# Optimization experiments

Measured on AMD Instinct MI355X. Metric: run time of the kernel, lower is better.

The kernel has to match this reference:

```python
import jax, jax.numpy as jnp
import numpy as np

BOOST_STRENGTH = 1.0  # from init kwargs, already >= 0


def setup_inputs() -> dict:
    key = jax.random.key(0)
    k1, k2 = jax.random.split(key)
    B, C, H, W = 64, 128, 56, 56
    x = jax.random.normal(k1, (B, C, H, W), dtype=jnp.float32)
    # duty cycles are running activation frequencies in [0, 1]
    duty_cycles = jax.random.uniform(k2, (1, C, 1, 1), dtype=jnp.float32)
    k = 40141  # round(0.1 * C*H*W)
    return {"x": x, "duty_cycles": duty_cycles, "k": k}


def reference(x, duty_cycles, k):
    B = x.shape[0]
    n = x.shape[1] * x.shape[2] * x.shape[3]
    target_density = jnp.float32(k / n)
    # boosting only selects winners; original (unboosted) values are kept
    boost_factors = jnp.exp((target_density - duty_cycles) * BOOST_STRENGTH)
    boosted = (x * boost_factors).reshape(B, -1)   # [B, n]
    flat_x = x.reshape(B, -1)                      # [B, n]
    _, idx = jax.lax.top_k(boosted, k)             # [B, k]
    winners = jnp.take_along_axis(flat_x, idx, axis=1)  # original values at winning units
    res = jnp.zeros_like(flat_x).at[jnp.arange(B)[:, None], idx].set(winners)
    return res.reshape(x.shape)
```

## Files before the change

kernel.cpp:

```cpp
#include <hip/hip_runtime.h>
#include <stdint.h>

#define BB 64
#define CC 128
#define HW 3136
#define NPR (CC * HW)
#define NBINS 8192
#define BIN_SHIFT 19
#define KEY_LOW 0x7FFFFu
#define NF4 6272
#define F4CH 784

typedef float vf4 __attribute__((ext_vector_type(4)));

#define ROWMETA_OFF 512
#define COUNTER_OFF 2048
#define HIST_OFF 4096
#define CAND_OFF (HIST_OFF + (size_t)BB * NBINS * 4)

__device__ __forceinline__ uint32_t tokey(float b) {
    uint32_t u = __float_as_uint(b);
    return u ^ (uint32_t)(((int32_t)u >> 31) | 0x80000000);
}

__device__ __forceinline__ float boostf(const float* dc, int c, int K) {
    float td = (float)((double)K / (double)NPR);
    float d = td - dc[c];
    return (float)exp((double)d);
}

__global__ __launch_bounds__(256) void k_hist(const float* __restrict__ x,
                                              const float* __restrict__ dc,
                                              const int* __restrict__ kptr,
                                              uint32_t* __restrict__ hist) {
    __shared__ uint32_t lh[NBINS];
    __shared__ float sbf[8];
    for (int i = threadIdx.x; i < NBINS; i += 256) lh[i] = 0;
    if (threadIdx.x < 8) {
        int c0 = (blockIdx.x & 15) * 8;
        sbf[threadIdx.x] = boostf(dc, c0 + threadIdx.x, *kptr);
    }
    __syncthreads();

    int row = blockIdx.x >> 4;
    int c0 = (blockIdx.x & 15) * 8;
    const float4* xp = (const float4*)(x + (size_t)row * NPR + (size_t)c0 * HW);

#define HPROC(av, tv)                                             \
    do {                                                          \
        float f_ = sbf[(tv) / F4CH];                              \
        atomicAdd(&lh[tokey((av).x * f_) >> BIN_SHIFT], 1u);      \
        atomicAdd(&lh[tokey((av).y * f_) >> BIN_SHIFT], 1u);      \
        atomicAdd(&lh[tokey((av).z * f_) >> BIN_SHIFT], 1u);      \
        atomicAdd(&lh[tokey((av).w * f_) >> BIN_SHIFT], 1u);      \
    } while (0)

    const int tid = threadIdx.x;
    float4 c0v = xp[tid];
    float4 c1v = xp[tid + 256];
    float4 c2v = xp[tid + 512];
    float4 c3v = xp[tid + 768];
    int tcur = tid;
    #pragma unroll
    for (int g = 1; g < 6; ++g) {
        int tn = g * 1024 + tid;
        float4 n0 = xp[tn];
        float4 n1 = xp[tn + 256];
        float4 n2 = xp[tn + 512];
        float4 n3 = xp[tn + 768];
        HPROC(c0v, tcur);
        HPROC(c1v, tcur + 256);
        HPROC(c2v, tcur + 512);
        HPROC(c3v, tcur + 768);
        c0v = n0; c1v = n1; c2v = n2; c3v = n3;
        tcur = tn;
    }
    HPROC(c0v, tcur);
    HPROC(c1v, tcur + 256);
    HPROC(c2v, tcur + 512);
    HPROC(c3v, tcur + 768);
    if (tid < 128) {
        float4 a = xp[6144 + tid];
        HPROC(a, 6144 + tid);
    }
#undef HPROC

    __syncthreads();
    uint32_t* gh = hist + (size_t)row * NBINS;
    for (int i = threadIdx.x; i < NBINS; i += 256) {
        uint32_t v = lh[i];
        if (v) atomicAdd(&gh[i], v);
    }
}

__global__ __launch_bounds__(256) void k_write_scan(const float* __restrict__ x,
                                                    const float* __restrict__ dc,
                                                    const int* __restrict__ kptr,
                                                    const uint32_t* __restrict__ hist,
                                                    int2* __restrict__ rowmeta,
                                                    float* __restrict__ out,
                                                    unsigned long long* __restrict__ cand,
                                                    uint32_t* __restrict__ counters,
                                                    int cap) {
    const int tid = threadIdx.x;
    const int row = blockIdx.x >> 4;
    const int c0 = (blockIdx.x & 15) * 8;
    const int K = *kptr;

    __shared__ float sbf[8];
    __shared__ uint32_t lcnt, gbase;
    __shared__ unsigned long long lbuf[2048];
    __shared__ uint32_t csum[256];
    __shared__ int2 smeta;
    if (tid == 0) lcnt = 0;
    if (tid < 8) sbf[tid] = boostf(dc, c0 + tid, K);

    {
        const uint32_t* gh = hist + (size_t)row * NBINS;
        uint32_t Ku = (uint32_t)K;
        int hi = NBINS - 1 - 32 * tid;
        uint32_t hv[32];
        #pragma unroll
        for (int j = 0; j < 32; j++) hv[j] = gh[hi - j];
        uint32_t ssum = 0;
        #pragma unroll
        for (int j = 0; j < 32; j++) ssum += hv[j];
        csum[tid] = ssum;
        __syncthreads();
        for (int off = 1; off < 256; off <<= 1) {
            uint32_t v = (tid >= off) ? csum[tid - off] : 0u;
            __syncthreads();
            csum[tid] += v;
            __syncthreads();
        }
        uint32_t incl = csum[tid];
        uint32_t excl = incl - ssum;
        if (excl < Ku && incl >= Ku) {
            uint32_t cum = excl;
            #pragma unroll
            for (int j = 0; j < 32; j++) {
                if (cum + hv[j] >= Ku) { smeta = make_int2(hi - j, (int)(Ku - cum)); break; }
                cum += hv[j];
            }
        }
        __syncthreads();
    }
    const int bstar = smeta.x;
    if (tid == 0 && (blockIdx.x & 15) == 0) rowmeta[row] = smeta;

    size_t base = (size_t)row * NPR + (size_t)c0 * HW;
    const float4* xp = (const float4*)(x + base);
    vf4* op = (vf4*)(out + base);
    int jbase = c0 * HW;

#define PROC4(av, tu)                                                            \
    do {                                                                         \
        float fv = sbf[(tu) / F4CH];                                             \
        vf4 oa;                                                                  \
        float* ai = (float*)&(av);                                               \
        _Pragma("unroll")                                                        \
        for (int q = 0; q < 4; q++) {                                            \
            float xv = ai[q];                                                    \
            uint32_t key = tokey(xv * fv);                                       \
            int bin = (int)(key >> BIN_SHIFT);                                   \
            oa[q] = (bin > bstar) ? xv : 0.0f;                                   \
            if (bin == bstar) {                                                  \
                uint32_t j = (uint32_t)(jbase + 4 * (tu) + q);                   \
                unsigned long long packed =                                      \
                    ((unsigned long long)(key & KEY_LOW) << 32) | (uint32_t)(~j);\
                uint32_t pos = atomicAdd(&lcnt, 1u);                             \
                if (pos < 2048u) lbuf[pos] = packed;                             \
                else {                                                           \
                    uint32_t gp = atomicAdd(&counters[row], 1u);                 \
                    if ((int)gp < cap) cand[(size_t)row * cap + gp] = packed;    \
                }                                                                \
            }                                                                    \
        }                                                                        \
        __builtin_nontemporal_store(oa, &op[(tu)]);                              \
    } while (0)

    float4 c0v = xp[tid];
    float4 c1v = xp[tid + 256];
    float4 c2v = xp[tid + 512];
    float4 c3v = xp[tid + 768];
    int tcur = tid;
    #pragma unroll
    for (int g = 1; g < 6; ++g) {
        int tn = g * 1024 + tid;
        float4 n0 = xp[tn];
        float4 n1 = xp[tn + 256];
        float4 n2 = xp[tn + 512];
        float4 n3 = xp[tn + 768];
        PROC4(c0v, tcur);
        PROC4(c1v, tcur + 256);
        PROC4(c2v, tcur + 512);
        PROC4(c3v, tcur + 768);
        c0v = n0; c1v = n1; c2v = n2; c3v = n3;
        tcur = tn;
    }
    PROC4(c0v, tcur);
    PROC4(c1v, tcur + 256);
    PROC4(c2v, tcur + 512);
    PROC4(c3v, tcur + 768);
    if (tid < 128) {
        float4 a = xp[6144 + tid];
        PROC4(a, 6144 + tid);
    }
#undef PROC4

    __syncthreads();
    uint32_t m = lcnt < 2048u ? lcnt : 2048u;
    if (tid == 0) gbase = atomicAdd(&counters[row], m);
    __syncthreads();
    for (uint32_t i = tid; i < m; i += 256) {
        uint32_t pos = gbase + i;
        if ((int)pos < cap) cand[(size_t)row * cap + pos] = lbuf[i];
    }
}

__global__ __launch_bounds__(1024) void k_select(const float* __restrict__ x,
                                                 float* __restrict__ out,
                                                 const unsigned long long* __restrict__ cand,
                                                 const uint32_t* __restrict__ counters,
                                                 const int2* __restrict__ rowmeta,
                                                 int cap) {
    int row = blockIdx.x;
    uint32_t cnt = counters[row];
    if ((int)cnt > cap) cnt = (uint32_t)cap;
    int E = rowmeta[row].y;
    const unsigned long long* cp = cand + (size_t)row * cap;
    int tid = threadIdx.x;

    __shared__ uint32_t hist[256];
    __shared__ uint32_t sufs[256];
    __shared__ unsigned long long buf[6144];
    __shared__ uint32_t scnt;
    __shared__ int sh_d, sh_done;

    unsigned long long prefix = 0ull, mask = 0ull, thr = 0ull;
    uint32_t remaining = (uint32_t)E;
    bool compacted = false;
    uint32_t csize = cnt;
    if (tid == 0) sh_done = 0;

    for (int shift = 48; shift >= 0; shift -= 8) {
        if (tid < 256) hist[tid] = 0;
        __syncthreads();
        if (!compacted) {
            for (uint32_t s = tid; s < cnt; s += 1024) {
                unsigned long long v = cp[s];
                if ((v & mask) == prefix)
                    atomicAdd(&hist[(uint32_t)(v >> shift) & 255u], 1u);
            }
        } else {
            for (uint32_t s = tid; s < csize; s += 1024)
                atomicAdd(&hist[(uint32_t)(buf[s] >> shift) & 255u], 1u);
        }
        __syncthreads();
        if (tid < 256) sufs[tid] = hist[tid];
        __syncthreads();
        for (int off = 1; off < 256; off <<= 1) {
            uint32_t add = 0;
            if (tid < 256 && tid + off < 256) add = sufs[tid + off];
            __syncthreads();
            if (tid < 256) sufs[tid] += add;
            __syncthreads();
        }
        if (tid < 256) {
            uint32_t sd = sufs[tid];
            uint32_t sn = (tid < 255) ? sufs[tid + 1] : 0u;
            if (sd >= remaining && sn < remaining) sh_d = tid;
        }
        __syncthreads();
        int d = sh_d;
        uint32_t cumG = (d < 255) ? sufs[d + 1] : 0u;
        uint32_t binC = sufs[d] - cumG;
        unsigned long long npref = prefix | ((unsigned long long)(uint32_t)d << shift);
        unsigned long long nmask = mask | (0xFFull << shift);
        bool done = (sufs[d] == remaining);
        if (done) {
            thr = npref;
            if (tid == 0) sh_done = 1;
        }
        remaining -= cumG;
        __syncthreads();
        if (!sh_done && binC <= 6144u && shift > 0) {
            if (tid == 0) scnt = 0;
            __syncthreads();
            for (uint32_t s = tid; s < cnt; s += 1024) {
                unsigned long long v = cp[s];
                if ((v & nmask) == npref) {
                    uint32_t p = atomicAdd(&scnt, 1u);
                    buf[p] = v;
                }
            }
            __syncthreads();
            csize = binC;
            compacted = true;
        }
        prefix = npref;
        mask = nmask;
        if (sh_done) break;
    }
    if (!sh_done) thr = prefix;

    const float* xr = x + (size_t)row * NPR;
    float* orow = out + (size_t)row * NPR;
    for (uint32_t s = tid; s < cnt; s += 1024) {
        unsigned long long v = cp[s];
        if (v >= thr) {
            uint32_t j = ~(uint32_t)v;
            orow[j] = xr[j];
        }
    }
}

extern "C" void kernel_launch(void* const* d_in, const int* in_sizes, int n_in,
                              void* d_out, int out_size, void* d_ws, size_t ws_size,
                              hipStream_t stream) {
    const float* x  = (const float*)d_in[0];
    const float* dc = (const float*)d_in[1];
    const int* kptr = (const int*)d_in[2];
    float* out = (float*)d_out;

    char* ws = (char*)d_ws;
    int2* rowmeta       = (int2*)(ws + ROWMETA_OFF);
    uint32_t* counters  = (uint32_t*)(ws + COUNTER_OFF);
    uint32_t* hist      = (uint32_t*)(ws + HIST_OFF);
    unsigned long long* cand = (unsigned long long*)(ws + CAND_OFF);

    size_t cap_sz = (ws_size > CAND_OFF) ? (ws_size - CAND_OFF) / ((size_t)BB * 8) : 0;
    if (cap_sz > 65536) cap_sz = 65536;
    int cap = (int)cap_sz;

    (void)hipMemsetAsync(ws, 0, CAND_OFF, stream);
    k_hist<<<BB * 16, 256, 0, stream>>>(x, dc, kptr, hist);
    k_write_scan<<<BB * 16, 256, 0, stream>>>(x, dc, kptr, hist, rowmeta, out,
                                              cand, counters, cap);
    k_select<<<BB, 1024, 0, stream>>>(x, out, cand, counters, rowmeta, cap);
}
```

Before: 222.7 us.

## Split rows into 32 channel groups, pack histogram to 16-bit bins, batch loads

Both streaming kernels now launch twice as many blocks, each covering 4 channels instead of 8, which doubles the grid to 2048 blocks for better occupancy and latency hiding. The histogram kernel packs two 16-bit counters per 32-bit shared word, halving LDS use to raise occupancy. Both kernels now issue all 12 float4 loads up front instead of a rolling double buffer. The costs are more global atomic merges of the per-block histograms and higher register pressure from the 12 outstanding loads.

Measured after the change: 223.8 us. No clear change (+0.5%).

```diff
diff --git a/kernel.cpp b/kernel.cpp
--- a/kernel.cpp
+++ b/kernel.cpp
@@ -8,7 +8,9 @@
 #define NBINS 8192
 #define BIN_SHIFT 19
 #define KEY_LOW 0x7FFFFu
-#define NF4 6272
+#define GROUPS 32
+#define GCH 4
+#define NF4 3136
 #define F4CH 784
 
 typedef float vf4 __attribute__((ext_vector_type(4)));
@@ -33,63 +35,50 @@
                                               const float* __restrict__ dc,
                                               const int* __restrict__ kptr,
                                               uint32_t* __restrict__ hist) {
-    __shared__ uint32_t lh[NBINS];
-    __shared__ float sbf[8];
-    for (int i = threadIdx.x; i < NBINS; i += 256) lh[i] = 0;
-    if (threadIdx.x < 8) {
-        int c0 = (blockIdx.x & 15) * 8;
-        sbf[threadIdx.x] = boostf(dc, c0 + threadIdx.x, *kptr);
+    __shared__ uint32_t lh32[NBINS / 2];
+    __shared__ float sbf[GCH];
+    const int tid = threadIdx.x;
+    for (int i = tid; i < NBINS / 2; i += 256) lh32[i] = 0;
+    if (tid < GCH) {
+        int c0 = (blockIdx.x & (GROUPS - 1)) * GCH;
+        sbf[tid] = boostf(dc, c0 + tid, *kptr);
     }
     __syncthreads();
 
-    int row = blockIdx.x >> 4;
-    int c0 = (blockIdx.x & 15) * 8;
+    const int row = blockIdx.x >> 5;
+    const int c0 = (blockIdx.x & (GROUPS - 1)) * GCH;
     const float4* xp = (const float4*)(x + (size_t)row * NPR + (size_t)c0 * HW);
 
-#define HPROC(av, tv)                                             \
-    do {                                                          \
-        float f_ = sbf[(tv) / F4CH];                              \
-        atomicAdd(&lh[tokey((av).x * f_) >> BIN_SHIFT], 1u);      \
-        atomicAdd(&lh[tokey((av).y * f_) >> BIN_SHIFT], 1u);      \
-        atomicAdd(&lh[tokey((av).z * f_) >> BIN_SHIFT], 1u);      \
-        atomicAdd(&lh[tokey((av).w * f_) >> BIN_SHIFT], 1u);      \
+#define HPROC(av, tv)                                                          \
+    do {                                                                       \
+        float f_ = sbf[(tv) / F4CH];                                           \
+        uint32_t b_;                                                           \
+        b_ = tokey((av).x * f_) >> BIN_SHIFT;                                  \
+        atomicAdd(&lh32[b_ >> 1], 1u << ((b_ & 1) << 4));                      \
+        b_ = tokey((av).y * f_) >> BIN_SHIFT;                                  \
+        atomicAdd(&lh32[b_ >> 1], 1u << ((b_ & 1) << 4));                      \
+        b_ = tokey((av).z * f_) >> BIN_SHIFT;                                  \
+        atomicAdd(&lh32[b_ >> 1], 1u << ((b_ & 1) << 4));                      \
+        b_ = tokey((av).w * f_) >> BIN_SHIFT;                                  \
+        atomicAdd(&lh32[b_ >> 1], 1u << ((b_ & 1) << 4));                      \
     } while (0)
 
-    const int tid = threadIdx.x;
-    float4 c0v = xp[tid];
-    float4 c1v = xp[tid + 256];
-    float4 c2v = xp[tid + 512];
-    float4 c3v = xp[tid + 768];
-    int tcur = tid;
+    float4 v[12];
     #pragma unroll
-    for (int g = 1; g < 6; ++g) {
-        int tn = g * 1024 + tid;
-        float4 n0 = xp[tn];
-        float4 n1 = xp[tn + 256];
-        float4 n2 = xp[tn + 512];
-        float4 n3 = xp[tn + 768];
-        HPROC(c0v, tcur);
-        HPROC(c1v, tcur + 256);
-        HPROC(c2v, tcur + 512);
-        HPROC(c3v, tcur + 768);
-        c0v = n0; c1v = n1; c2v = n2; c3v = n3;
-        tcur = tn;
-    }
-    HPROC(c0v, tcur);
-    HPROC(c1v, tcur + 256);
-    HPROC(c2v, tcur + 512);
-    HPROC(c3v, tcur + 768);
-    if (tid < 128) {
-        float4 a = xp[6144 + tid];
-        HPROC(a, 6144 + tid);
-    }
+    for (int g = 0; g < 12; ++g) v[g] = xp[tid + 256 * g];
+    float4 tl;
+    if (tid < 64) tl = xp[3072 + tid];
+    #pragma unroll
+    for (int g = 0; g < 12; ++g) HPROC(v[g], tid + 256 * g);
+    if (tid < 64) HPROC(tl, 3072 + tid);
 #undef HPROC
 
     __syncthreads();
     uint32_t* gh = hist + (size_t)row * NBINS;
-    for (int i = threadIdx.x; i < NBINS; i += 256) {
-        uint32_t v = lh[i];
-        if (v) atomicAdd(&gh[i], v);
+    for (int i = tid; i < NBINS / 2; i += 256) {
+        uint32_t w = lh32[i];
+        if (w & 0xFFFFu) atomicAdd(&gh[2 * i], w & 0xFFFFu);
+        if (w >> 16)     atomicAdd(&gh[2 * i + 1], w >> 16);
     }
 }
 
@@ -103,17 +92,17 @@
                                                     uint32_t* __restrict__ counters,
                                                     int cap) {
     const int tid = threadIdx.x;
-    const int row = blockIdx.x >> 4;
-    const int c0 = (blockIdx.x & 15) * 8;
+    const int row = blockIdx.x >> 5;
+    const int c0 = (blockIdx.x & (GROUPS - 1)) * GCH;
     const int K = *kptr;
 
-    __shared__ float sbf[8];
+    __shared__ float sbf[GCH];
     __shared__ uint32_t lcnt, gbase;
     __shared__ unsigned long long lbuf[2048];
     __shared__ uint32_t csum[256];
     __shared__ int2 smeta;
     if (tid == 0) lcnt = 0;
-    if (tid < 8) sbf[tid] = boostf(dc, c0 + tid, K);
+    if (tid < GCH) sbf[tid] = boostf(dc, c0 + tid, K);
 
     {
         const uint32_t* gh = hist + (size_t)row * NBINS;
@@ -146,7 +135,7 @@
         __syncthreads();
     }
     const int bstar = smeta.x;
-    if (tid == 0 && (blockIdx.x & 15) == 0) rowmeta[row] = smeta;
+    if (tid == 0 && (blockIdx.x & (GROUPS - 1)) == 0) rowmeta[row] = smeta;
 
     size_t base = (size_t)row * NPR + (size_t)c0 * HW;
     const float4* xp = (const float4*)(x + base);
@@ -179,33 +168,14 @@
         __builtin_nontemporal_store(oa, &op[(tu)]);                              \
     } while (0)
 
-    float4 c0v = xp[tid];
-    float4 c1v = xp[tid + 256];
-    float4 c2v = xp[tid + 512];
-    float4 c3v = xp[tid + 768];
-    int tcur = tid;
+    float4 v[12];
     #pragma unroll
-    for (int g = 1; g < 6; ++g) {
-        int tn = g * 1024 + tid;
-        float4 n0 = xp[tn];
-        float4 n1 = xp[tn + 256];
-        float4 n2 = xp[tn + 512];
-        float4 n3 = xp[tn + 768];
-        PROC4(c0v, tcur);
-        PROC4(c1v, tcur + 256);
-        PROC4(c2v, tcur + 512);
-        PROC4(c3v, tcur + 768);
-        c0v = n0; c1v = n1; c2v = n2; c3v = n3;
-        tcur = tn;
-    }
-    PROC4(c0v, tcur);
-    PROC4(c1v, tcur + 256);
-    PROC4(c2v, tcur + 512);
-    PROC4(c3v, tcur + 768);
-    if (tid < 128) {
-        float4 a = xp[6144 + tid];
-        PROC4(a, 6144 + tid);
-    }
+    for (int g = 0; g < 12; ++g) v[g] = xp[tid + 256 * g];
+    float4 tl;
+    if (tid < 64) tl = xp[3072 + tid];
+    #pragma unroll
+    for (int g = 0; g < 12; ++g) PROC4(v[g], tid + 256 * g);
+    if (tid < 64) PROC4(tl, 3072 + tid);
 #undef PROC4
 
     __syncthreads();
@@ -334,8 +304,8 @@
     int cap = (int)cap_sz;
 
     (void)hipMemsetAsync(ws, 0, CAND_OFF, stream);
-    k_hist<<<BB * 16, 256, 0, stream>>>(x, dc, kptr, hist);
-    k_write_scan<<<BB * 16, 256, 0, stream>>>(x, dc, kptr, hist, rowmeta, out,
-                                              cand, counters, cap);
+    k_hist<<<BB * GROUPS, 256, 0, stream>>>(x, dc, kptr, hist);
+    k_write_scan<<<BB * GROUPS, 256, 0, stream>>>(x, dc, kptr, hist, rowmeta, out,
+                                                  cand, counters, cap);
     k_select<<<BB, 1024, 0, stream>>>(x, out, cand, counters, rowmeta, cap);
 }
```
